# Kernel tuning notes

Measured on AMD Instinct MI355X. Metric: run time of the kernel, lower is better.

## Reference

```python
import jax, jax.numpy as jnp
import numpy as np

N = 100000      # nodes
E = 1600000     # edges
F_IN = 128      # n_feat
AGG = 48        # agg_hidden
FC = 192        # fc_hidden
NC = 10         # n_class
ED = 4          # edge_dim
SLOPE = 0.2     # GATv2 LeakyReLU negative slope
N_LAYER = 3


def _glorot(k, shape):
    fan = shape[-1]
    return (jax.random.normal(k, shape, jnp.float32) / np.sqrt(fan)).astype(jnp.float32)


def setup_inputs() -> dict:
    key = jax.random.key(0)
    ks = jax.random.split(key, 40)
    inp = {}
    inp["x"] = jax.random.normal(ks[0], (N, F_IN), jnp.float32)
    inp["edge_index"] = jax.random.randint(ks[1], (2, E), 0, N)
    inp["edge_attr"] = jax.random.normal(ks[2], (E, ED), jnp.float32)
    dims = [F_IN, AGG, AGG]
    i = 3
    for l in range(N_LAYER):
        d = dims[l]
        inp[f"Wl{l}"] = _glorot(ks[i], (AGG, d)); i += 1   # lin_l weight
        inp[f"bl{l}"] = jnp.zeros((AGG,), jnp.float32)
        inp[f"Wr{l}"] = _glorot(ks[i], (AGG, d)); i += 1   # lin_r weight
        inp[f"br{l}"] = jnp.zeros((AGG,), jnp.float32)
        inp[f"We{l}"] = _glorot(ks[i], (AGG, ED)); i += 1  # lin_edge weight (no bias)
        inp[f"att{l}"] = _glorot(ks[i], (AGG,)); i += 1    # attention vector a
        inp[f"b{l}"] = jnp.zeros((AGG,), jnp.float32)      # output bias
    inp["fc1_w"] = _glorot(ks[i], (FC, AGG)); i += 1
    inp["fc1_b"] = jnp.zeros((FC,), jnp.float32)
    inp["fc2_w"] = _glorot(ks[i], (NC, FC)); i += 1
    inp["fc2_b"] = jnp.zeros((NC,), jnp.float32)
    return inp


def _gatv2(x, src, dst, ea, Wl, bl, Wr, br, We, att, b):
    # GATv2Conv, heads=1, concat=True, eval mode (dropout off)
    xl = x @ Wl.T + bl                                   # [N, AGG] source transform
    xr = x @ Wr.T + br                                   # [N, AGG] target transform
    m = jax.nn.leaky_relu(xl[src] + xr[dst] + ea @ We.T, SLOPE)  # [E, AGG]
    e = m @ att                                          # [E] attention logits
    # segment softmax over incoming edges of each destination node
    emax = jax.ops.segment_max(e, dst, num_segments=N)
    ee = jnp.exp(e - emax[dst])
    den = jax.ops.segment_sum(ee, dst, num_segments=N)
    alpha = ee / jnp.maximum(den, 1e-16)[dst]            # [E]
    out = jax.ops.segment_sum(alpha[:, None] * xl[src], dst, num_segments=N)
    return out + b


def reference(x, edge_index, edge_attr,
              Wl0, bl0, Wr0, br0, We0, att0, b0,
              Wl1, bl1, Wr1, br1, We1, att1, b1,
              Wl2, bl2, Wr2, br2, We2, att2, b2,
              fc1_w, fc1_b, fc2_w, fc2_b):
    src, dst = edge_index[0], edge_index[1]
    layers = [
        (Wl0, bl0, Wr0, br0, We0, att0, b0),
        (Wl1, bl1, Wr1, br1, We1, att1, b1),
        (Wl2, bl2, Wr2, br2, We2, att2, b2),
    ]
    h = x
    for p in layers:
        h = jax.nn.relu(_gatv2(h, src, dst, edge_attr, *p))
    g = jnp.sum(h, axis=0)                               # readout='sum' -> [AGG]
    g = jax.nn.relu(g @ fc1_w.T + fc1_b)                 # [FC]
    return jax.nn.softmax(g @ fc2_w.T + fc2_b)           # [NC]
```

## Files before the change

### kernel.cpp

```cpp
#include <hip/hip_runtime.h>
#include <hip/hip_fp16.h>
#include <math.h>

#define NNODE 100000
#define NEDGE 1600000
#define FIN   128
#define AGG   48
#define FCH   192
#define NCLS  10
#define SLOPE 0.2f
#define L2E   1.44269504088896340736f

#define NBUCK 391
#define BCAP  4992

__device__ __forceinline__ float2 h2f(int p) {
    union { int i; __half2 h; } u; u.i = p;
    return __half22float2(u.h);
}
__device__ __forceinline__ int f2h(float a, float b) {
    union { __half2 h; int i; } u;
    u.h = __floats2half2_rn(a, b);
    return u.i;
}


__global__ __launch_bounds__(256) void binA_kernel(const int* __restrict__ ei,
                                                   const float4* __restrict__ ea,
                                                   int* __restrict__ deg,
                                                   int* __restrict__ bcnt,
                                                   int4* __restrict__ bbuf) {
    __shared__ int hist[NBUCK];
    __shared__ int base[NBUCK];
    const int t = threadIdx.x;
    const int wgbase = blockIdx.x * 4096;
    for (int i = t; i < NBUCK; i += 256) hist[i] = 0;
    __syncthreads();

    int d[16], rank[16];
#pragma unroll
    for (int i = 0; i < 16; ++i) {
        int e = wgbase + i * 256 + t;
        if (e < NEDGE) {
            d[i] = ei[NEDGE + e];
            rank[i] = atomicAdd(&hist[d[i] >> 8], 1);
            atomicAdd(&deg[d[i]], 1);
        } else {
            d[i] = -1;
            rank[i] = 0;
        }
    }
    __syncthreads();
    for (int i = t; i < NBUCK; i += 256)
        base[i] = hist[i] ? atomicAdd(&bcnt[i], hist[i]) : 0;
    __syncthreads();

#pragma unroll
    for (int i = 0; i < 16; ++i) {
        int e = wgbase + i * 256 + t;
        if (e < NEDGE) {
            int b = d[i] >> 8;
            int pos = base[b] + rank[i];
            if (pos < BCAP) {
                float4 v = ea[e];
                bbuf[(size_t)b * BCAP + pos] =
                    make_int4(ei[e], d[i], f2h(v.x, v.y), f2h(v.z, v.w));
            }
        }
    }
}

__global__ void scan1_kernel(const int* __restrict__ deg, int* __restrict__ starts,
                             int* __restrict__ bsum) {
    __shared__ int s[256];
    int t = threadIdx.x;
    int i = blockIdx.x * 256 + t;
    int v = (i < NNODE) ? deg[i] : 0;
    s[t] = v;
    __syncthreads();
    int acc = v;
    for (int o = 1; o < 256; o <<= 1) {
        int x = (t >= o) ? s[t - o] : 0;
        __syncthreads();
        acc += x;
        s[t] = acc;
        __syncthreads();
    }
    if (i < NNODE) starts[i] = acc - v;
    if (t == 255) bsum[blockIdx.x] = acc;
}

__global__ void scan2_kernel(int* __restrict__ bsum, int nb) {
    __shared__ int s[512];
    int t = threadIdx.x;
    int v = (t < nb) ? bsum[t] : 0;
    s[t] = v;
    __syncthreads();
    int acc = v;
    for (int o = 1; o < 512; o <<= 1) {
        int x = (t >= o) ? s[t - o] : 0;
        __syncthreads();
        acc += x;
        s[t] = acc;
        __syncthreads();
    }
    if (t < nb) bsum[t] = acc - v;
}

__global__ void scan3_kernel(int* __restrict__ starts, const int* __restrict__ bsum) {
    int i = blockIdx.x * 256 + threadIdx.x;
    if (i < NNODE) starts[i] += bsum[blockIdx.x];
    if (i == 0) starts[NNODE] = NEDGE;
}

__global__ __launch_bounds__(256) void binB_kernel(const int* __restrict__ bcnt,
                                                   const int4* __restrict__ bbuf,
                                                   const int* __restrict__ starts,
                                                   int4* __restrict__ edges) {
    __shared__ int lcur[256];
    const int b = blockIdx.x;
    const int t = threadIdx.x;
    int node = (b << 8) + t;
    lcur[t] = (node < NNODE) ? starts[node] : 0;
    __syncthreads();
    int cnt = bcnt[b];
    if (cnt > BCAP) cnt = BCAP;
    for (int i = t; i < cnt; i += 256) {
        int4 rec = bbuf[(size_t)b * BCAP + i];
        int pos = atomicAdd(&lcur[rec.y & 255], 1);
        edges[pos] = make_int4(rec.x, rec.z, rec.w, 0);
    }
}


template <int K>
__global__ __launch_bounds__(192) void transform_tiled(
    const float* __restrict__ h,
    const float* __restrict__ Wl, const float* __restrict__ bl,
    const float* __restrict__ Wr, const float* __restrict__ br,
    __half* __restrict__ xlh, float* __restrict__ xr)
{
    constexpr int NT = 48;
    constexpr int KP = K + 1;
    __shared__ float sWl[K * 48];
    __shared__ float sWr[K * 48];
    __shared__ float sH[NT * KP];

    const int t = threadIdx.x;
    const int base = blockIdx.x * NT;

    for (int idx = t; idx < 48 * K; idx += 192) {
        int k = idx / K;
        int j = idx - k * K;
        sWl[j * 48 + k] = Wl[idx];
        sWr[j * 48 + k] = Wr[idx];
    }
    for (int p = t; p < NT * (K / 4); p += 192) {
        int row = p / (K / 4);
        int c4  = p - row * (K / 4);
        int gn  = base + row;
        float4 v = (gn < NNODE) ? ((const float4*)h)[(size_t)gn * (K / 4) + c4]
                                : make_float4(0.f, 0.f, 0.f, 0.f);
        float* d = &sH[row * KP + c4 * 4];
        d[0] = v.x; d[1] = v.y; d[2] = v.z; d[3] = v.w;
    }
    __syncthreads();

    const int q  = t % 12;
    const int ng = t / 12;
    float al[3][4] = {};
    float ar[3][4] = {};

    const float4* sWl4 = (const float4*)sWl;
    const float4* sWr4 = (const float4*)sWr;
#pragma unroll 4
    for (int j = 0; j < K; ++j) {
        float4 wl4 = sWl4[j * 12 + q];
        float4 wr4 = sWr4[j * 12 + q];
        float h0 = sH[(ng + 0)  * KP + j];
        float h1 = sH[(ng + 16) * KP + j];
        float h2 = sH[(ng + 32) * KP + j];
        al[0][0] += h0 * wl4.x; al[0][1] += h0 * wl4.y; al[0][2] += h0 * wl4.z; al[0][3] += h0 * wl4.w;
        ar[0][0] += h0 * wr4.x; ar[0][1] += h0 * wr4.y; ar[0][2] += h0 * wr4.z; ar[0][3] += h0 * wr4.w;
        al[1][0] += h1 * wl4.x; al[1][1] += h1 * wl4.y; al[1][2] += h1 * wl4.z; al[1][3] += h1 * wl4.w;
        ar[1][0] += h1 * wr4.x; ar[1][1] += h1 * wr4.y; ar[1][2] += h1 * wr4.z; ar[1][3] += h1 * wr4.w;
        al[2][0] += h2 * wl4.x; al[2][1] += h2 * wl4.y; al[2][2] += h2 * wl4.z; al[2][3] += h2 * wl4.w;
        ar[2][0] += h2 * wr4.x; ar[2][1] += h2 * wr4.y; ar[2][2] += h2 * wr4.z; ar[2][3] += h2 * wr4.w;
    }

    float4 bl4 = ((const float4*)bl)[q];
    float4 br4 = ((const float4*)br)[q];
#pragma unroll
    for (int i = 0; i < 3; ++i) {
        int gn = base + ng + 16 * i;
        if (gn < NNODE) {
            int2 pk = make_int2(f2h(al[i][0] + bl4.x, al[i][1] + bl4.y),
                                f2h(al[i][2] + bl4.z, al[i][3] + bl4.w));
            ((int2*)xlh)[(size_t)gn * 16 + q] = pk;
            float4 orr = make_float4(ar[i][0] + br4.x, ar[i][1] + br4.y,
                                     ar[i][2] + br4.z, ar[i][3] + br4.w);
            ((float4*)xr)[(size_t)gn * 12 + q] = orr;
        }
    }
}

__device__ __forceinline__ float group_sum16(float v) {
#define DPP_ADD(ctrl)                                                          \
    v += __int_as_float(__builtin_amdgcn_update_dpp(                           \
        0, __float_as_int(v), ctrl, 0xf, 0xf, true))
    DPP_ADD(0xB1);
    DPP_ADD(0x4E);
    DPP_ADD(0x141);
    DPP_ADD(0x140);
#undef DPP_ADD
    return v;
}

__global__ void aggregate_kernel(const __half* __restrict__ xlh, const float* __restrict__ xr,
                                 const int* __restrict__ starts, const int4* __restrict__ edges,
                                 const float* __restrict__ We, const float* __restrict__ att,
                                 const float* __restrict__ bias,
                                 float* __restrict__ hout) {
    int node = (blockIdx.x * blockDim.x + threadIdx.x) >> 6;
    if (node >= NNODE) return;
    const int lane = threadIdx.x & 63;
    const int g = lane >> 4;
    const int r = lane & 15;
    const bool act = r < 12;
    const int rc = act ? r : 0;

    const float4* We4 = (const float4*)We;
    float4 w0 = We4[4 * rc + 0], w1 = We4[4 * rc + 1],
           w2 = We4[4 * rc + 2], w3 = We4[4 * rc + 3];
    float4 a4 = ((const float4*)att)[rc];
    float aA = act ? a4.x * L2E : 0.f;
    float aB = act ? a4.y * L2E : 0.f;
    float aC = act ? a4.z * L2E : 0.f;
    float aD = act ? a4.w * L2E : 0.f;
    float4 xr4 = ((const float4*)xr)[(size_t)node * 12 + rc];

    int s = starts[node];
    int e_end = starts[node + 1];
    float den = 0.f, ac0 = 0.f, ac1 = 0.f, ac2 = 0.f, ac3 = 0.f;

    for (int j = s; j < e_end; j += 8) {
        int j0 = j + g, j1 = j + 4 + g;
        bool v0 = j0 < e_end, v1 = j1 < e_end;
        int4 edA = edges[v0 ? j0 : j];
        int4 edB = edges[v1 ? j1 : j];
        int2 xiA = ((const int2*)xlh)[(size_t)edA.x * 16 + rc];
        int2 xiB = ((const int2*)xlh)[(size_t)edB.x * 16 + rc];

        float2 eA01 = h2f(edA.y), eA23 = h2f(edA.z);
        float2 eB01 = h2f(edB.y), eB23 = h2f(edB.z);
        float2 xA01 = h2f(xiA.x), xA23 = h2f(xiA.y);
        float2 xB01 = h2f(xiB.x), xB23 = h2f(xiB.y);

        float vA0 = fmaf(w0.w, eA23.y, fmaf(w0.z, eA23.x, fmaf(w0.y, eA01.y, fmaf(w0.x, eA01.x, xA01.x + xr4.x))));
        float vA1 = fmaf(w1.w, eA23.y, fmaf(w1.z, eA23.x, fmaf(w1.y, eA01.y, fmaf(w1.x, eA01.x, xA01.y + xr4.y))));
        float vA2 = fmaf(w2.w, eA23.y, fmaf(w2.z, eA23.x, fmaf(w2.y, eA01.y, fmaf(w2.x, eA01.x, xA23.x + xr4.z))));
        float vA3 = fmaf(w3.w, eA23.y, fmaf(w3.z, eA23.x, fmaf(w3.y, eA01.y, fmaf(w3.x, eA01.x, xA23.y + xr4.w))));
        float vB0 = fmaf(w0.w, eB23.y, fmaf(w0.z, eB23.x, fmaf(w0.y, eB01.y, fmaf(w0.x, eB01.x, xB01.x + xr4.x))));
        float vB1 = fmaf(w1.w, eB23.y, fmaf(w1.z, eB23.x, fmaf(w1.y, eB01.y, fmaf(w1.x, eB01.x, xB01.y + xr4.y))));
        float vB2 = fmaf(w2.w, eB23.y, fmaf(w2.z, eB23.x, fmaf(w2.y, eB01.y, fmaf(w2.x, eB01.x, xB23.x + xr4.z))));
        float vB3 = fmaf(w3.w, eB23.y, fmaf(w3.z, eB23.x, fmaf(w3.y, eB01.y, fmaf(w3.x, eB01.x, xB23.y + xr4.w))));

        float tA, tB;
        tA =           aA * fmaf(SLOPE, fminf(vA0, 0.f), fmaxf(vA0, 0.f));
        tA = fmaf(aB, fmaf(SLOPE, fminf(vA1, 0.f), fmaxf(vA1, 0.f)), tA);
        tA = fmaf(aC, fmaf(SLOPE, fminf(vA2, 0.f), fmaxf(vA2, 0.f)), tA);
        tA = fmaf(aD, fmaf(SLOPE, fminf(vA3, 0.f), fmaxf(vA3, 0.f)), tA);
        tB =           aA * fmaf(SLOPE, fminf(vB0, 0.f), fmaxf(vB0, 0.f));
        tB = fmaf(aB, fmaf(SLOPE, fminf(vB1, 0.f), fmaxf(vB1, 0.f)), tB);
        tB = fmaf(aC, fmaf(SLOPE, fminf(vB2, 0.f), fmaxf(vB2, 0.f)), tB);
        tB = fmaf(aD, fmaf(SLOPE, fminf(vB3, 0.f), fmaxf(vB3, 0.f)), tB);

        tA = group_sum16(tA);
        tB = group_sum16(tB);

        float pA = v0 ? exp2f(tA) : 0.f;
        float pB = v1 ? exp2f(tB) : 0.f;
        den += pA + pB;
        ac0 = fmaf(pB, xB01.x, fmaf(pA, xA01.x, ac0));
        ac1 = fmaf(pB, xB01.y, fmaf(pA, xA01.y, ac1));
        ac2 = fmaf(pB, xB23.x, fmaf(pA, xA23.x, ac2));
        ac3 = fmaf(pB, xB23.y, fmaf(pA, xA23.y, ac3));
    }

    den += __int_as_float(__builtin_amdgcn_ds_swizzle(__float_as_int(den), 0x401F));
    ac0 += __int_as_float(__builtin_amdgcn_ds_swizzle(__float_as_int(ac0), 0x401F));
    ac1 += __int_as_float(__builtin_amdgcn_ds_swizzle(__float_as_int(ac1), 0x401F));
    ac2 += __int_as_float(__builtin_amdgcn_ds_swizzle(__float_as_int(ac2), 0x401F));
    ac3 += __int_as_float(__builtin_amdgcn_ds_swizzle(__float_as_int(ac3), 0x401F));
    den += __shfl_xor(den, 32);
    ac0 += __shfl_xor(ac0, 32);
    ac1 += __shfl_xor(ac1, 32);
    ac2 += __shfl_xor(ac2, 32);
    ac3 += __shfl_xor(ac3, 32);

    if (lane < 16 && act) {
        float inv = 1.f / fmaxf(den, 1e-16f);
        float4 b4 = ((const float4*)bias)[r];
        float4 o = make_float4(fmaxf(fmaf(ac0, inv, b4.x), 0.f),
                               fmaxf(fmaf(ac1, inv, b4.y), 0.f),
                               fmaxf(fmaf(ac2, inv, b4.z), 0.f),
                               fmaxf(fmaf(ac3, inv, b4.w), 0.f));
        ((float4*)hout)[(size_t)node * 12 + r] = o;
    }
}


__global__ void readout_kernel(const float* __restrict__ h, float* __restrict__ g) {
    int wid = (blockIdx.x * blockDim.x + threadIdx.x) >> 6;
    int lane = threadIdx.x & 63;
    int nw = (gridDim.x * blockDim.x) >> 6;
    if (lane < AGG) {
        float acc = 0.f;
        for (int n = wid; n < NNODE; n += nw) acc += h[n * AGG + lane];
        atomicAdd(&g[lane], acc);
    }
}

__global__ void head_kernel(const float* __restrict__ g,
                            const float* __restrict__ fc1w, const float* __restrict__ fc1b,
                            const float* __restrict__ fc2w, const float* __restrict__ fc2b,
                            float* __restrict__ out) {
    __shared__ float sg[AGG];
    __shared__ float s1[FCH];
    __shared__ float s2[NCLS];
    int t = threadIdx.x;
    if (t < AGG) sg[t] = g[t];
    __syncthreads();
    if (t < FCH) {
        float a = fc1b[t];
        for (int j = 0; j < AGG; ++j) a += fc1w[t * AGG + j] * sg[j];
        s1[t] = fmaxf(a, 0.f);
    }
    __syncthreads();
    if (t < NCLS) {
        float a = fc2b[t];
        for (int j = 0; j < FCH; ++j) a += fc2w[t * FCH + j] * s1[j];
        s2[t] = a;
    }
    __syncthreads();
    if (t == 0) {
        float mx = s2[0];
        for (int i = 1; i < NCLS; ++i) mx = fmaxf(mx, s2[i]);
        float ex[NCLS];
        float den = 0.f;
        for (int i = 0; i < NCLS; ++i) { ex[i] = __expf(s2[i] - mx); den += ex[i]; }
        for (int i = 0; i < NCLS; ++i) out[i] = ex[i] / den;
    }
}


extern "C" void kernel_launch(void* const* d_in, const int* in_sizes, int n_in,
                              void* d_out, int out_size, void* d_ws, size_t ws_size,
                              hipStream_t stream) {
    const float* x  = (const float*)d_in[0];
    const int*   ei = (const int*)d_in[1];
    const float* ea = (const float*)d_in[2];
    const float* Wl[3], *bl[3], *Wr[3], *br[3], *We[3], *att[3], *bb[3];
    for (int l = 0; l < 3; ++l) {
        int base = 3 + l * 7;
        Wl[l]  = (const float*)d_in[base + 0];
        bl[l]  = (const float*)d_in[base + 1];
        Wr[l]  = (const float*)d_in[base + 2];
        br[l]  = (const float*)d_in[base + 3];
        We[l]  = (const float*)d_in[base + 4];
        att[l] = (const float*)d_in[base + 5];
        bb[l]  = (const float*)d_in[base + 6];
    }
    const float* fc1w = (const float*)d_in[24];
    const float* fc1b = (const float*)d_in[25];
    const float* fc2w = (const float*)d_in[26];
    const float* fc2b = (const float*)d_in[27];
    float* outp = (float*)d_out;

    char* ws = (char*)d_ws;
    __half* xlh   = (__half*)ws;
    float*  xr    = (float*)(ws + (size_t)NNODE * 64 * 2);
    int4*   bbuf  = (int4*)ws;
    size_t off = (size_t)NNODE * 64 * 2 + (size_t)NNODE * AGG * 4;
    auto take = [&](size_t bytes) -> void* {
        void* p = ws + off;
        off = (off + bytes + 255) & ~(size_t)255;
        return p;
    };
    float*  h      = (float*)take((size_t)NNODE * AGG * 4);
    int*    deg    = (int*)take((size_t)NNODE * 4);
    int*    starts = (int*)take((size_t)(NNODE + 1) * 4);
    int*    bsum   = (int*)take(1024 * 4);
    int*    bcnt   = (int*)take(NBUCK * 4);
    int4*   edges  = (int4*)take((size_t)NEDGE * 16);
    float*  g      = (float*)take(64 * 4);

    const int NB1 = (NNODE + 255) / 256;

    hipMemsetAsync(deg, 0, (size_t)NNODE * 4, stream);
    hipMemsetAsync(bcnt, 0, NBUCK * 4, stream);
    binA_kernel<<<(NEDGE + 4095) / 4096, 256, 0, stream>>>(ei, (const float4*)ea,
                                                           deg, bcnt, bbuf);
    scan1_kernel<<<NB1, 256, 0, stream>>>(deg, starts, bsum);
    scan2_kernel<<<1, 512, 0, stream>>>(bsum, NB1);
    scan3_kernel<<<NB1, 256, 0, stream>>>(starts, bsum);
    binB_kernel<<<NBUCK, 256, 0, stream>>>(bcnt, bbuf, starts, edges);

    const int TGRID = (NNODE + 47) / 48;
    const int AGRID = (NNODE + 3) / 4;

    transform_tiled<FIN><<<TGRID, 192, 0, stream>>>(x, Wl[0], bl[0], Wr[0], br[0], xlh, xr);
    aggregate_kernel<<<AGRID, 256, 0, stream>>>(xlh, xr, starts, edges,
                                                We[0], att[0], bb[0], h);
    transform_tiled<AGG><<<TGRID, 192, 0, stream>>>(h, Wl[1], bl[1], Wr[1], br[1], xlh, xr);
    aggregate_kernel<<<AGRID, 256, 0, stream>>>(xlh, xr, starts, edges,
                                                We[1], att[1], bb[1], h);
    transform_tiled<AGG><<<TGRID, 192, 0, stream>>>(h, Wl[2], bl[2], Wr[2], br[2], xlh, xr);
    aggregate_kernel<<<AGRID, 256, 0, stream>>>(xlh, xr, starts, edges,
                                                We[2], att[2], bb[2], h);

    hipMemsetAsync(g, 0, 64 * 4, stream);
    readout_kernel<<<256, 256, 0, stream>>>(h, g);
    head_kernel<<<1, 192, 0, stream>>>(g, fc1w, fc1b, fc2w, fc2b, outp);
}
```

Before: 500.1 us.

## Stage binned edges in LDS for coalesced bucket writes; widen binB blocks

The binning kernel now groups each block's edges by bucket in shared memory, using a local prefix scan over the bucket histogram, and then writes them to the global bucket buffer in contiguous runs instead of scattered 16-byte stores. Edges per block drop from 4096 to 2048 so the staging arrays fit in LDS. binB is launched with 1024 threads per bucket to raise parallelism during the scatter. In exchange there are extra barriers and a scan in binA, higher LDS use that may limit occupancy, and more contention on the shared-memory atomics in binB.

```diff
diff --git a/kernel.cpp b/kernel.cpp
--- a/kernel.cpp
+++ b/kernel.cpp
@@ -13,6 +13,7 @@
 
 #define NBUCK 391
 #define BCAP  4992
+#define EPB   2048
 
 __device__ __forceinline__ float2 h2f(int p) {
     union { int i; __half2 h; } u; u.i = p;
@@ -30,43 +31,71 @@
                                                    int* __restrict__ deg,
                                                    int* __restrict__ bcnt,
                                                    int4* __restrict__ bbuf) {
-    __shared__ int hist[NBUCK];
-    __shared__ int base[NBUCK];
+    __shared__ int  hist[NBUCK];
+    __shared__ int  lofs[NBUCK];
+    __shared__ int  gbase[NBUCK];
+    __shared__ int  scA[512], scB[512];
+    __shared__ int  gidx[EPB];
+    __shared__ int4 stage[EPB];
+
     const int t = threadIdx.x;
-    const int wgbase = blockIdx.x * 4096;
+    const int wgbase = blockIdx.x * EPB;
+    const int nvalid = min(EPB, NEDGE - wgbase);
+
     for (int i = t; i < NBUCK; i += 256) hist[i] = 0;
     __syncthreads();
 
-    int d[16], rank[16];
+    int d[8], rank[8];
 #pragma unroll
-    for (int i = 0; i < 16; ++i) {
+    for (int i = 0; i < 8; ++i) {
         int e = wgbase + i * 256 + t;
         if (e < NEDGE) {
             d[i] = ei[NEDGE + e];
             rank[i] = atomicAdd(&hist[d[i] >> 8], 1);
             atomicAdd(&deg[d[i]], 1);
-        } else {
-            d[i] = -1;
-            rank[i] = 0;
+        } else d[i] = -1;
+    }
+    __syncthreads();
+
+    {
+        scA[t] = (t < NBUCK) ? hist[t] : 0;
+        scA[t + 256] = (t + 256 < NBUCK) ? hist[t + 256] : 0;
+        __syncthreads();
+        int* src = scA; int* dst = scB;
+#pragma unroll
+        for (int o = 1; o < 512; o <<= 1) {
+            int i0 = t, i1 = t + 256;
+            int v0 = src[i0] + ((i0 >= o) ? src[i0 - o] : 0);
+            int v1 = src[i1] + ((i1 >= o) ? src[i1 - o] : 0);
+            __syncthreads();
+            dst[i0] = v0; dst[i1] = v1;
+            __syncthreads();
+            int* tmp = src; src = dst; dst = tmp;
         }
-    }
-    __syncthreads();
+        if (t < NBUCK) lofs[t] = src[t] - hist[t];
+        if (t + 256 < NBUCK) lofs[t + 256] = src[t + 256] - hist[t + 256];
+    }
     for (int i = t; i < NBUCK; i += 256)
-        base[i] = hist[i] ? atomicAdd(&bcnt[i], hist[i]) : 0;
+        gbase[i] = hist[i] ? atomicAdd(&bcnt[i], hist[i]) : 0;
     __syncthreads();
 
 #pragma unroll
-    for (int i = 0; i < 16; ++i) {
+    for (int i = 0; i < 8; ++i) {
         int e = wgbase + i * 256 + t;
         if (e < NEDGE) {
             int b = d[i] >> 8;
-            int pos = base[b] + rank[i];
-            if (pos < BCAP) {
-                float4 v = ea[e];
-                bbuf[(size_t)b * BCAP + pos] =
-                    make_int4(ei[e], d[i], f2h(v.x, v.y), f2h(v.z, v.w));
-            }
+            int slot = lofs[b] + rank[i];
+            int gp = gbase[b] + rank[i];
+            float4 v = ea[e];
+            stage[slot] = make_int4(ei[e], d[i], f2h(v.x, v.y), f2h(v.z, v.w));
+            gidx[slot] = (gp < BCAP) ? (b * BCAP + gp) : -1;
         }
+    }
+    __syncthreads();
+
+    for (int i = t; i < nvalid; i += 256) {
+        int gi = gidx[i];
+        if (gi >= 0) bbuf[gi] = stage[i];
     }
 }
 
@@ -113,19 +142,21 @@
     if (i == 0) starts[NNODE] = NEDGE;
 }
 
-__global__ __launch_bounds__(256) void binB_kernel(const int* __restrict__ bcnt,
-                                                   const int4* __restrict__ bbuf,
-                                                   const int* __restrict__ starts,
-                                                   int4* __restrict__ edges) {
+__global__ __launch_bounds__(1024) void binB_kernel(const int* __restrict__ bcnt,
+                                                    const int4* __restrict__ bbuf,
+                                                    const int* __restrict__ starts,
+                                                    int4* __restrict__ edges) {
     __shared__ int lcur[256];
     const int b = blockIdx.x;
     const int t = threadIdx.x;
-    int node = (b << 8) + t;
-    lcur[t] = (node < NNODE) ? starts[node] : 0;
+    if (t < 256) {
+        int node = (b << 8) + t;
+        lcur[t] = (node < NNODE) ? starts[node] : 0;
+    }
     __syncthreads();
     int cnt = bcnt[b];
     if (cnt > BCAP) cnt = BCAP;
-    for (int i = t; i < cnt; i += 256) {
+    for (int i = t; i < cnt; i += 1024) {
         int4 rec = bbuf[(size_t)b * BCAP + i];
         int pos = atomicAdd(&lcur[rec.y & 255], 1);
         edges[pos] = make_int4(rec.x, rec.z, rec.w, 0);
@@ -399,12 +430,12 @@
 
     hipMemsetAsync(deg, 0, (size_t)NNODE * 4, stream);
     hipMemsetAsync(bcnt, 0, NBUCK * 4, stream);
-    binA_kernel<<<(NEDGE + 4095) / 4096, 256, 0, stream>>>(ei, (const float4*)ea,
-                                                           deg, bcnt, bbuf);
+    binA_kernel<<<(NEDGE + EPB - 1) / EPB, 256, 0, stream>>>(ei, (const float4*)ea,
+                                                             deg, bcnt, bbuf);
     scan1_kernel<<<NB1, 256, 0, stream>>>(deg, starts, bsum);
     scan2_kernel<<<1, 512, 0, stream>>>(bsum, NB1);
     scan3_kernel<<<NB1, 256, 0, stream>>>(starts, bsum);
-    binB_kernel<<<NBUCK, 256, 0, stream>>>(bcnt, bbuf, starts, edges);
+    binB_kernel<<<NBUCK, 1024, 0, stream>>>(bcnt, bbuf, starts, edges);
 
     const int TGRID = (NNODE + 47) / 48;
     const int AGRID = (NNODE + 3) / 4;
```

Result: no change. 510.0 us (+2.0%).
